# Kernel optimization log

Hardware: AMD Instinct MI355X
Metric: run time of the kernel (lower is better)

The kernel has to match this reference:

```python
import jax, jax.numpy as jnp
import numpy as np

N_NODES = 100000
N_EDGES = 1250000
D_IN = 64
D_H = 64
D_OUT = 32


def setup_inputs() -> dict:
    key = jax.random.key(0)
    ks = jax.random.split(key, 8)
    x = jax.random.normal(ks[0], (N_NODES, D_IN), dtype=jnp.float32)
    edge_index = jax.random.randint(ks[1], (2, N_EDGES), 0, N_NODES, dtype=jnp.int64)
    s = 0.1
    W1_l = jax.random.normal(ks[2], (D_H, D_IN), dtype=jnp.float32) * s
    W1_r = jax.random.normal(ks[3], (D_H, D_IN), dtype=jnp.float32) * s
    b1 = jnp.zeros((D_H,), dtype=jnp.float32)
    W2_l = jax.random.normal(ks[4], (D_OUT, D_H), dtype=jnp.float32) * s
    W2_r = jax.random.normal(ks[5], (D_OUT, D_H), dtype=jnp.float32) * s
    b2 = jnp.zeros((D_OUT,), dtype=jnp.float32)
    return {"x": x, "edge_index": edge_index, "W1_l": W1_l, "W1_r": W1_r,
            "b1": b1, "W2_l": W2_l, "W2_r": W2_r, "b2": b2}


def _sage_conv(x, src, dst, W_l, W_r, b):
    # PyG SAGEConv (aggr='mean', root_weight=True):
    #   out = lin_l(mean_{j in N(i)} x_j) + lin_r(x_i)
    n = x.shape[0]
    msg = x[src]                                            # [E, d] gather
    ssum = jax.ops.segment_sum(msg, dst, num_segments=n)    # [N, d]
    deg = jax.ops.segment_sum(jnp.ones((src.shape[0], 1), x.dtype), dst,
                              num_segments=n)               # [N, 1]
    mean = ssum / jnp.maximum(deg, 1.0)
    return mean @ W_l.T + b + x @ W_r.T


def reference(x, edge_index, W1_l, W1_r, b1, W2_l, W2_r, b2):
    src = edge_index[0]
    dst = edge_index[1]
    h = jax.nn.relu(_sage_conv(x, src, dst, W1_l, W1_r, b1))
    out = _sage_conv(h, src, dst, W2_l, W2_r, b2)
    return out
```

## Files before the change

### kernel.cpp

```cpp
#include <hip/hip_runtime.h>

#define N_NODES 100000
#define N_EDGES 1250000
#define D_IN 64
#define D_H 64
#define D_OUT 32

#define BUCKETS 196
#define GRP 512
#define PREP_NB 512
#define PREP_CH 2442
#define SCAP 48
#define BSTRIDE (PREP_NB*SCAP)
#define CSRCAP 8192

typedef __attribute__((ext_vector_type(8))) short bf16x8;
typedef __attribute__((ext_vector_type(4))) float f32x4;

__device__ __forceinline__ unsigned short f2bf(float f) {
    unsigned u = __float_as_uint(f);
    u = (u + 0x7fffu + ((u >> 16) & 1u)) >> 16;
    return (unsigned short)u;
}
__device__ __forceinline__ float bfhi(unsigned v) { return __uint_as_float(v & 0xffff0000u); }
__device__ __forceinline__ float bflo(unsigned v) { return __uint_as_float(v << 16); }


__global__ __launch_bounds__(256) void k_prep(const float* __restrict__ x,
                                              unsigned short* __restrict__ xh,
                                              const int* __restrict__ src,
                                              const int* __restrict__ dst,
                                              int* __restrict__ ebuf,
                                              int* __restrict__ pcnt) {
    __shared__ int ofs[BUCKETS];
    int t = threadIdx.x, b = blockIdx.x;
    for (int i = t; i < BUCKETS; i += 256) ofs[i] = 0;
    __syncthreads();

    const int TOT = N_NODES * 64 / 4;
    for (int i = b * 256 + t; i < TOT; i += PREP_NB * 256) {
        float4 v = *(const float4*)(x + (size_t)i * 4);
        uint2 u;
        u.x = (unsigned)f2bf(v.x) | ((unsigned)f2bf(v.y) << 16);
        u.y = (unsigned)f2bf(v.z) | ((unsigned)f2bf(v.w) << 16);
        *(uint2*)(xh + (size_t)i * 4) = u;
    }

    int e0 = b * PREP_CH;
    int e1 = e0 + PREP_CH; if (e1 > N_EDGES) e1 = N_EDGES;
    for (int e = e0 + t; e < e1; e += 256) {
        int s = src[e], d = dst[e];
        if ((unsigned)d >= N_NODES) continue;
        int sv = ((unsigned)s < N_NODES) ? s : 0;
        int bk = d >> 9;
        int r = atomicAdd(&ofs[bk], 1);
        if (r < SCAP) ebuf[bk * BSTRIDE + b * SCAP + r] = ((d & 511) << 17) | sv;
    }
    __syncthreads();
    for (int i = t; i < BUCKETS; i += 256) {
        int v = ofs[i]; if (v > SCAP) v = SCAP;
        pcnt[i * PREP_NB + b] = v;
    }
}

__global__ __launch_bounds__(512) void k_phb(const int* __restrict__ ebuf,
                                             const int* __restrict__ pcnt,
                                             int2* __restrict__ rd,
                                             int* __restrict__ csr_src) {
    __shared__ int sedge[CSRCAP];
    __shared__ int cnt[GRP];
    __shared__ int wsum[8];
    int b = blockIdx.x, t = threadIdx.x;
    int lane = t & 63, w = t >> 6;

    cnt[t] = 0;
    int c = pcnt[b * PREP_NB + t];

    int run = c;
    #pragma unroll
    for (int off = 1; off < 64; off <<= 1) {
        int u = __shfl_up(run, off, 64);
        if (lane >= off) run += u;
    }
    if (lane == 63) wsum[w] = run;
    __syncthreads();
    int wbase = 0, tot = 0;
    #pragma unroll
    for (int i = 0; i < 8; ++i) { int v = wsum[i]; tot += v; if (i < w) wbase += v; }
    int base = wbase + run - c;
    int n = tot; if (n > CSRCAP) n = CSRCAP;

    {
        const int4* sp4 = (const int4*)(ebuf + (size_t)b * BSTRIDE + (size_t)t * SCAP);
        for (int j = 0; j < c; j += 4) {
            int4 v = sp4[j >> 2];
            int p = base + j;
            if (p + 0 < CSRCAP)          sedge[p + 0] = v.x;
            if (j + 1 < c && p + 1 < CSRCAP) sedge[p + 1] = v.y;
            if (j + 2 < c && p + 2 < CSRCAP) sedge[p + 2] = v.z;
            if (j + 3 < c && p + 3 < CSRCAP) sedge[p + 3] = v.w;
        }
    }
    __syncthreads();
    for (int i = t; i < n; i += 512) atomicAdd(&cnt[sedge[i] >> 17], 1);
    __syncthreads();

    int d = cnt[t];
    int rund = d;
    #pragma unroll
    for (int off = 1; off < 64; off <<= 1) {
        int u = __shfl_up(rund, off, 64);
        if (lane >= off) rund += u;
    }
    if (lane == 63) wsum[w] = rund;
    __syncthreads();
    int wb2 = 0;
    #pragma unroll
    for (int i = 0; i < 8; ++i) { if (i < w) wb2 += wsum[i]; }
    int gabs = b * CSRCAP + wb2 + rund - d;
    int node = b * GRP + t;
    if (node < N_NODES) rd[node] = make_int2(gabs, d);
    cnt[t] = gabs;
    __syncthreads();
    for (int i = t; i < n; i += 512) {
        int v = sedge[i];
        int pos = atomicAdd(&cnt[v >> 17], 1);
        csr_src[pos] = v & 0x1FFFF;
    }
}

__global__ __launch_bounds__(256) void k_gather1(
    const unsigned short* __restrict__ xh,
    const int2* __restrict__ rd,
    const int* __restrict__ csr_src,
    unsigned int* __restrict__ meanh)
{
    int lane = threadIdx.x & 63;
    int wv = threadIdx.x >> 6;
    int c = lane & 31;
    int hb = lane & 32;
    const unsigned* xp = (const unsigned*)xh;

    int node0 = blockIdx.x * 8 + wv * 2 + (hb >> 5);
    for (int row = node0; row < N_NODES; row += gridDim.x * 8) {
        int2 rdv = rd[row];
        int start = rdv.x, dg = rdv.y;
        int end = start + dg;
        float x0 = 0.f, y0 = 0.f, x1 = 0.f, y1 = 0.f;
        float x2 = 0.f, y2 = 0.f, x3 = 0.f, y3 = 0.f;
        float x4 = 0.f, y4 = 0.f, x5 = 0.f, y5 = 0.f;
        float x6 = 0.f, y6 = 0.f, x7 = 0.f, y7 = 0.f;
        for (int eb = start; eb < end; eb += 32) {
            int nv = end - eb; if (nv > 32) nv = 32;
            int sid = (c < nv) ? csr_src[eb + c] : 0;
            int j = 0;
            for (; j + 8 <= nv; j += 8) {
                int s0 = __shfl(sid, hb + j + 0, 64);
                int s1 = __shfl(sid, hb + j + 1, 64);
                int s2 = __shfl(sid, hb + j + 2, 64);
                int s3 = __shfl(sid, hb + j + 3, 64);
                int s4 = __shfl(sid, hb + j + 4, 64);
                int s5 = __shfl(sid, hb + j + 5, 64);
                int s6 = __shfl(sid, hb + j + 6, 64);
                int s7 = __shfl(sid, hb + j + 7, 64);
                unsigned v0 = xp[s0 * 32 + c];
                unsigned v1 = xp[s1 * 32 + c];
                unsigned v2 = xp[s2 * 32 + c];
                unsigned v3 = xp[s3 * 32 + c];
                unsigned v4 = xp[s4 * 32 + c];
                unsigned v5 = xp[s5 * 32 + c];
                unsigned v6 = xp[s6 * 32 + c];
                unsigned v7 = xp[s7 * 32 + c];
                x0 += bflo(v0); y0 += bfhi(v0);
                x1 += bflo(v1); y1 += bfhi(v1);
                x2 += bflo(v2); y2 += bfhi(v2);
                x3 += bflo(v3); y3 += bfhi(v3);
                x4 += bflo(v4); y4 += bfhi(v4);
                x5 += bflo(v5); y5 += bfhi(v5);
                x6 += bflo(v6); y6 += bfhi(v6);
                x7 += bflo(v7); y7 += bfhi(v7);
            }
            for (; j + 4 <= nv; j += 4) {
                int s0 = __shfl(sid, hb + j + 0, 64);
                int s1 = __shfl(sid, hb + j + 1, 64);
                int s2 = __shfl(sid, hb + j + 2, 64);
                int s3 = __shfl(sid, hb + j + 3, 64);
                unsigned v0 = xp[s0 * 32 + c];
                unsigned v1 = xp[s1 * 32 + c];
                unsigned v2 = xp[s2 * 32 + c];
                unsigned v3 = xp[s3 * 32 + c];
                x0 += bflo(v0); y0 += bfhi(v0);
                x1 += bflo(v1); y1 += bfhi(v1);
                x2 += bflo(v2); y2 += bfhi(v2);
                x3 += bflo(v3); y3 += bfhi(v3);
            }
            for (; j < nv; ++j) {
                int s = __shfl(sid, hb + j, 64);
                unsigned v = xp[s * 32 + c];
                x0 += bflo(v); y0 += bfhi(v);
            }
        }
        float rdeg = 1.0f / fmaxf((float)dg, 1.0f);
        float fx = (((x0 + x1) + (x2 + x3)) + ((x4 + x5) + (x6 + x7))) * rdeg;
        float fy = (((y0 + y1) + (y2 + y3)) + ((y4 + y5) + (y6 + y7))) * rdeg;
        meanh[(size_t)row * 32 + c] = (unsigned)f2bf(fx) | ((unsigned)f2bf(fy) << 16);
    }
}

__global__ __launch_bounds__(256) void k_gemm1(
    const unsigned short* __restrict__ xh, const unsigned short* __restrict__ meanh,
    const float* __restrict__ W1l, const float* __restrict__ W1r,
    const float* __restrict__ b1,
    const float* __restrict__ W2l, const float* __restrict__ W2r,
    unsigned short* __restrict__ hWlh, unsigned short* __restrict__ hrh)
{
    __shared__ short sWB1[4 * 4 * 64 * 8];
    __shared__ short sWB2[2 * 4 * 64 * 8];
    __shared__ short htile[4][16 * 72];

    int tid = threadIdx.x;
    for (int e = tid; e < 1024; e += 256) {
        int kc = e >> 8, nt = (e >> 6) & 3, ln = e & 63;
        int cc = ln & 15, qd = ln >> 4;
        int n = nt * 16 + cc, k0 = kc * 32 + qd * 8;
        const float* sp = (k0 < 64) ? (W1l + n * 64 + k0) : (W1r + n * 64 + (k0 - 64));
        short* dp = sWB1 + e * 8;
        #pragma unroll
        for (int j = 0; j < 8; ++j) dp[j] = (short)f2bf(sp[j]);
    }
    for (int e = tid; e < 512; e += 256) {
        int kc = e >> 8, nt = (e >> 6) & 3, ln = e & 63;
        int cc = ln & 15, qd = ln >> 4;
        int n = nt * 16 + cc, k0 = kc * 32 + qd * 8;
        const float* sp = (n < 32) ? (W2l + n * 64 + k0) : (W2r + (n - 32) * 64 + k0);
        short* dp = sWB2 + e * 8;
        #pragma unroll
        for (int j = 0; j < 8; ++j) dp[j] = (short)f2bf(sp[j]);
    }
    __syncthreads();

    int lane = tid & 63, w = tid >> 6;
    int c = lane & 15, quad = lane >> 4;
    float bias[4];
    #pragma unroll
    for (int nt = 0; nt < 4; ++nt) bias[nt] = b1[nt * 16 + c];

    const bf16x8* B1 = (const bf16x8*)sWB1;
    const bf16x8* B2 = (const bf16x8*)sWB2;
    short* ht = htile[w];

    for (int r0 = blockIdx.x * 64 + w * 16; r0 < N_NODES; r0 += gridDim.x * 64) {
        int ra = r0 + c; if (ra > N_NODES - 1) ra = N_NODES - 1;
        const bf16x8* mrow = (const bf16x8*)(meanh + (size_t)ra * 64);
        const bf16x8* xrow = (const bf16x8*)(xh + (size_t)ra * 64);
        bf16x8 a0 = mrow[quad];
        bf16x8 a1 = mrow[4 + quad];
        bf16x8 a2 = xrow[quad];
        bf16x8 a3 = xrow[4 + quad];

        f32x4 acc[4];
        #pragma unroll
        for (int nt = 0; nt < 4; ++nt) acc[nt] = (f32x4){0.f, 0.f, 0.f, 0.f};
        #pragma unroll
        for (int nt = 0; nt < 4; ++nt)
            acc[nt] = __builtin_amdgcn_mfma_f32_16x16x32_bf16(a0, B1[(0 * 4 + nt) * 64 + lane], acc[nt], 0, 0, 0);
        #pragma unroll
        for (int nt = 0; nt < 4; ++nt)
            acc[nt] = __builtin_amdgcn_mfma_f32_16x16x32_bf16(a1, B1[(1 * 4 + nt) * 64 + lane], acc[nt], 0, 0, 0);
        #pragma unroll
        for (int nt = 0; nt < 4; ++nt)
            acc[nt] = __builtin_amdgcn_mfma_f32_16x16x32_bf16(a2, B1[(2 * 4 + nt) * 64 + lane], acc[nt], 0, 0, 0);
        #pragma unroll
        for (int nt = 0; nt < 4; ++nt)
            acc[nt] = __builtin_amdgcn_mfma_f32_16x16x32_bf16(a3, B1[(3 * 4 + nt) * 64 + lane], acc[nt], 0, 0, 0);

        #pragma unroll
        for (int nt = 0; nt < 4; ++nt) {
            #pragma unroll
            for (int reg = 0; reg < 4; ++reg) {
                float hv = fmaxf(acc[nt][reg] + bias[nt], 0.0f);
                ht[(quad * 4 + reg) * 72 + nt * 16 + c] = (short)f2bf(hv);
            }
        }
        bf16x8 h0 = *(const bf16x8*)(ht + c * 72 + 0  + quad * 8);
        bf16x8 h1 = *(const bf16x8*)(ht + c * 72 + 32 + quad * 8);

        f32x4 acc2[4];
        #pragma unroll
        for (int nt = 0; nt < 4; ++nt) acc2[nt] = (f32x4){0.f, 0.f, 0.f, 0.f};
        #pragma unroll
        for (int nt = 0; nt < 4; ++nt)
            acc2[nt] = __builtin_amdgcn_mfma_f32_16x16x32_bf16(h0, B2[(0 * 4 + nt) * 64 + lane], acc2[nt], 0, 0, 0);
        #pragma unroll
        for (int nt = 0; nt < 4; ++nt)
            acc2[nt] = __builtin_amdgcn_mfma_f32_16x16x32_bf16(h1, B2[(1 * 4 + nt) * 64 + lane], acc2[nt], 0, 0, 0);

        #pragma unroll
        for (int nt = 0; nt < 4; ++nt) {
            #pragma unroll
            for (int reg = 0; reg < 4; ++reg) {
                int row = r0 + quad * 4 + reg;
                if (row < N_NODES) {
                    unsigned short q = f2bf(acc2[nt][reg]);
                    if (nt < 2) hWlh[(size_t)row * 32 + nt * 16 + c] = q;
                    else        hrh [(size_t)row * 32 + (nt - 2) * 16 + c] = q;
                }
            }
        }
    }
}

__global__ __launch_bounds__(256) void k_l2(
    const unsigned short* __restrict__ hWlh, const unsigned short* __restrict__ hrh,
    const int2* __restrict__ rd,
    const int* __restrict__ csr_src,
    const float* __restrict__ b2, float* __restrict__ out)
{
    int lane = threadIdx.x & 63;
    int wv = threadIdx.x >> 6;
    int c = lane & 15;
    int qb = lane & 48;
    const unsigned* hp  = (const unsigned*)hWlh;
    const unsigned* hrp = (const unsigned*)hrh;
    float2 b2v = ((const float2*)b2)[c];

    int node0 = blockIdx.x * 16 + wv * 4 + (qb >> 4);
    for (int row = node0; row < N_NODES; row += gridDim.x * 16) {
        int2 rdv = rd[row];
        int start = rdv.x, dg = rdv.y;
        int end = start + dg;
        float x0 = 0.f, y0 = 0.f, x1 = 0.f, y1 = 0.f;
        float x2 = 0.f, y2 = 0.f, x3 = 0.f, y3 = 0.f;
        float x4 = 0.f, y4 = 0.f, x5 = 0.f, y5 = 0.f;
        float x6 = 0.f, y6 = 0.f, x7 = 0.f, y7 = 0.f;
        for (int eb = start; eb < end; eb += 16) {
            int nv = end - eb; if (nv > 16) nv = 16;
            int sid = (c < nv) ? csr_src[eb + c] : 0;
            int j = 0;
            for (; j + 8 <= nv; j += 8) {
                int s0 = __shfl(sid, qb + j + 0, 64);
                int s1 = __shfl(sid, qb + j + 1, 64);
                int s2 = __shfl(sid, qb + j + 2, 64);
                int s3 = __shfl(sid, qb + j + 3, 64);
                int s4 = __shfl(sid, qb + j + 4, 64);
                int s5 = __shfl(sid, qb + j + 5, 64);
                int s6 = __shfl(sid, qb + j + 6, 64);
                int s7 = __shfl(sid, qb + j + 7, 64);
                unsigned v0 = hp[s0 * 16 + c];
                unsigned v1 = hp[s1 * 16 + c];
                unsigned v2 = hp[s2 * 16 + c];
                unsigned v3 = hp[s3 * 16 + c];
                unsigned v4 = hp[s4 * 16 + c];
                unsigned v5 = hp[s5 * 16 + c];
                unsigned v6 = hp[s6 * 16 + c];
                unsigned v7 = hp[s7 * 16 + c];
                x0 += bflo(v0); y0 += bfhi(v0);
                x1 += bflo(v1); y1 += bfhi(v1);
                x2 += bflo(v2); y2 += bfhi(v2);
                x3 += bflo(v3); y3 += bfhi(v3);
                x4 += bflo(v4); y4 += bfhi(v4);
                x5 += bflo(v5); y5 += bfhi(v5);
                x6 += bflo(v6); y6 += bfhi(v6);
                x7 += bflo(v7); y7 += bfhi(v7);
            }
            for (; j + 4 <= nv; j += 4) {
                int s0 = __shfl(sid, qb + j + 0, 64);
                int s1 = __shfl(sid, qb + j + 1, 64);
                int s2 = __shfl(sid, qb + j + 2, 64);
                int s3 = __shfl(sid, qb + j + 3, 64);
                unsigned v0 = hp[s0 * 16 + c];
                unsigned v1 = hp[s1 * 16 + c];
                unsigned v2 = hp[s2 * 16 + c];
                unsigned v3 = hp[s3 * 16 + c];
                x0 += bflo(v0); y0 += bfhi(v0);
                x1 += bflo(v1); y1 += bfhi(v1);
                x2 += bflo(v2); y2 += bfhi(v2);
                x3 += bflo(v3); y3 += bfhi(v3);
            }
            for (; j < nv; ++j) {
                int s = __shfl(sid, qb + j, 64);
                unsigned v = hp[s * 16 + c];
                x0 += bflo(v); y0 += bfhi(v);
            }
        }
        float fx = ((x0 + x1) + (x2 + x3)) + ((x4 + x5) + (x6 + x7));
        float fy = ((y0 + y1) + (y2 + y3)) + ((y4 + y5) + (y6 + y7));
        float rdeg = 1.0f / fmaxf((float)dg, 1.0f);
        unsigned hru = hrp[(size_t)row * 16 + c];
        float2 o;
        o.x = fmaf(fx, rdeg, bflo(hru) + b2v.x);
        o.y = fmaf(fy, rdeg, bfhi(hru) + b2v.y);
        ((float2*)out)[(size_t)row * 16 + c] = o;
    }
}

extern "C" void kernel_launch(void* const* d_in, const int* in_sizes, int n_in,
                              void* d_out, int out_size, void* d_ws, size_t ws_size,
                              hipStream_t stream) {
    const float* x   = (const float*)d_in[0];
    const int*   ei  = (const int*)d_in[1];
    const float* W1l = (const float*)d_in[2];
    const float* W1r = (const float*)d_in[3];
    const float* b1  = (const float*)d_in[4];
    const float* W2l = (const float*)d_in[5];
    const float* W2r = (const float*)d_in[6];
    const float* b2  = (const float*)d_in[7];
    float* out = (float*)d_out;

    const int* src = ei;
    const int* dst = ei + N_EDGES;

    char* w = (char*)d_ws;
    int2* rd     = (int2*)w;  w += sizeof(int2) * (N_NODES + 4);
    int* pcnt    = (int*)w;   w += sizeof(int) * (PREP_NB * BUCKETS);
    int* csr_src = (int*)w;   w += sizeof(int) * (BUCKETS * CSRCAP);
    int* ebuf    = (int*)w;   w += sizeof(int) * ((size_t)BUCKETS * BSTRIDE);
    unsigned short* xh    = (unsigned short*)w; w += sizeof(short) * (size_t)N_NODES * 64;
    unsigned int*   meanh = (unsigned int*)w;   w += sizeof(int)   * (size_t)N_NODES * 32;
    unsigned short* hWlh  = (unsigned short*)w; w += sizeof(short) * (size_t)N_NODES * 32;
    unsigned short* hrh   = (unsigned short*)w;

    k_prep<<<PREP_NB, 256, 0, stream>>>(x, xh, src, dst, ebuf, pcnt);
    k_phb<<<BUCKETS, 512, 0, stream>>>(ebuf, pcnt, rd, csr_src);
    k_gather1<<<4096, 256, 0, stream>>>(xh, rd, csr_src, meanh);
    k_gemm1<<<(N_NODES + 63) / 64, 256, 0, stream>>>(
        xh, (const unsigned short*)meanh, W1l, W1r, b1, W2l, W2r, hWlh, hrh);
    k_l2<<<4096, 256, 0, stream>>>(hWlh, hrh, rd, csr_src, b2, out);
}
```

Baseline: 195.7 us.

## Quantize gathered node features to int8 with per-row scales for both aggregations

Per-row int8 quantization (offset by 128, with an fp32 scale) replaces the bf16 copies of x and of h·W2_l that the two neighbor-gather kernels read. Each gathered row shrinks from 128 to 64 bytes in layer 1 and from 64 to 32 bytes in layer 2, and the lane mapping is regrouped so each lane dequantizes four values per load. The intent is to cut random-access gather bandwidth, which dominates these kernels. In exchange it adds an extra per-edge scale load and shuffle, extra integer-to-float conversion arithmetic, and coarser 8-bit precision in the aggregated means.

```diff
diff --git a/kernel.cpp b/kernel.cpp
--- a/kernel.cpp
+++ b/kernel.cpp
@@ -28,6 +28,8 @@
 
 __global__ __launch_bounds__(256) void k_prep(const float* __restrict__ x,
                                               unsigned short* __restrict__ xh,
+                                              unsigned* __restrict__ xq,
+                                              float* __restrict__ xscale,
                                               const int* __restrict__ src,
                                               const int* __restrict__ dst,
                                               int* __restrict__ ebuf,
@@ -37,13 +39,25 @@
     for (int i = t; i < BUCKETS; i += 256) ofs[i] = 0;
     __syncthreads();
 
-    const int TOT = N_NODES * 64 / 4;
-    for (int i = b * 256 + t; i < TOT; i += PREP_NB * 256) {
-        float4 v = *(const float4*)(x + (size_t)i * 4);
-        uint2 u;
-        u.x = (unsigned)f2bf(v.x) | ((unsigned)f2bf(v.y) << 16);
-        u.y = (unsigned)f2bf(v.z) | ((unsigned)f2bf(v.w) << 16);
-        *(uint2*)(xh + (size_t)i * 4) = u;
+    int ql = t & 15;
+    for (int row = b * 16 + (t >> 4); row < N_NODES; row += PREP_NB * 16) {
+        float4 v = *(const float4*)(x + (size_t)row * 64 + ql * 4);
+        float amax = fmaxf(fmaxf(fabsf(v.x), fabsf(v.y)), fmaxf(fabsf(v.z), fabsf(v.w)));
+        amax = fmaxf(amax, __shfl_xor(amax, 1, 64));
+        amax = fmaxf(amax, __shfl_xor(amax, 2, 64));
+        amax = fmaxf(amax, __shfl_xor(amax, 4, 64));
+        amax = fmaxf(amax, __shfl_xor(amax, 8, 64));
+        float sinv = (amax > 0.f) ? 127.0f / amax : 0.f;
+        unsigned q0 = (unsigned)((int)rintf(v.x * sinv) + 128);
+        unsigned q1 = (unsigned)((int)rintf(v.y * sinv) + 128);
+        unsigned q2 = (unsigned)((int)rintf(v.z * sinv) + 128);
+        unsigned q3 = (unsigned)((int)rintf(v.w * sinv) + 128);
+        xq[(size_t)row * 16 + ql] = q0 | (q1 << 8) | (q2 << 16) | (q3 << 24);
+        if (ql == 0) xscale[row] = (amax > 0.f) ? amax / 127.0f : 0.f;
+        uint2 hb;
+        hb.x = (unsigned)f2bf(v.x) | ((unsigned)f2bf(v.y) << 16);
+        hb.y = (unsigned)f2bf(v.z) | ((unsigned)f2bf(v.w) << 16);
+        ((uint2*)xh)[(size_t)row * 16 + ql] = hb;
     }
 
     int e0 = b * PREP_CH;
@@ -95,7 +109,7 @@
         for (int j = 0; j < c; j += 4) {
             int4 v = sp4[j >> 2];
             int p = base + j;
-            if (p + 0 < CSRCAP)          sedge[p + 0] = v.x;
+            if (p + 0 < CSRCAP)              sedge[p + 0] = v.x;
             if (j + 1 < c && p + 1 < CSRCAP) sedge[p + 1] = v.y;
             if (j + 2 < c && p + 2 < CSRCAP) sedge[p + 2] = v.z;
             if (j + 3 < c && p + 3 < CSRCAP) sedge[p + 3] = v.w;
@@ -130,80 +144,79 @@
 }
 
 __global__ __launch_bounds__(256) void k_gather1(
-    const unsigned short* __restrict__ xh,
-    const int2* __restrict__ rd,
-    const int* __restrict__ csr_src,
-    unsigned int* __restrict__ meanh)
+    const unsigned* __restrict__ xq, const float* __restrict__ xscale,
+    const int2* __restrict__ rd, const int* __restrict__ csr_src,
+    uint2* __restrict__ meanh)
 {
     int lane = threadIdx.x & 63;
     int wv = threadIdx.x >> 6;
-    int c = lane & 31;
-    int hb = lane & 32;
-    const unsigned* xp = (const unsigned*)xh;
-
-    int node0 = blockIdx.x * 8 + wv * 2 + (hb >> 5);
-    for (int row = node0; row < N_NODES; row += gridDim.x * 8) {
+    int c = lane & 15;
+    int qb = lane & 48;
+
+    int node0 = blockIdx.x * 16 + wv * 4 + (qb >> 4);
+    for (int row = node0; row < N_NODES; row += gridDim.x * 16) {
         int2 rdv = rd[row];
         int start = rdv.x, dg = rdv.y;
         int end = start + dg;
-        float x0 = 0.f, y0 = 0.f, x1 = 0.f, y1 = 0.f;
-        float x2 = 0.f, y2 = 0.f, x3 = 0.f, y3 = 0.f;
-        float x4 = 0.f, y4 = 0.f, x5 = 0.f, y5 = 0.f;
-        float x6 = 0.f, y6 = 0.f, x7 = 0.f, y7 = 0.f;
-        for (int eb = start; eb < end; eb += 32) {
-            int nv = end - eb; if (nv > 32) nv = 32;
-            int sid = (c < nv) ? csr_src[eb + c] : 0;
+        float A0=0,A1=0,A2=0,A3=0, B0=0,B1=0,B2=0,B3=0;
+        float C0=0,C1=0,C2=0,C3=0, D0=0,D1=0,D2=0,D3=0;
+        float ss0=0, ss1=0, ss2=0, ss3=0;
+        for (int eb = start; eb < end; eb += 16) {
+            int nv = end - eb; if (nv > 16) nv = 16;
+            int sid = 0; float sc = 0.f;
+            if (c < nv) { sid = csr_src[eb + c]; sc = xscale[sid]; }
             int j = 0;
-            for (; j + 8 <= nv; j += 8) {
-                int s0 = __shfl(sid, hb + j + 0, 64);
-                int s1 = __shfl(sid, hb + j + 1, 64);
-                int s2 = __shfl(sid, hb + j + 2, 64);
-                int s3 = __shfl(sid, hb + j + 3, 64);
-                int s4 = __shfl(sid, hb + j + 4, 64);
-                int s5 = __shfl(sid, hb + j + 5, 64);
-                int s6 = __shfl(sid, hb + j + 6, 64);
-                int s7 = __shfl(sid, hb + j + 7, 64);
-                unsigned v0 = xp[s0 * 32 + c];
-                unsigned v1 = xp[s1 * 32 + c];
-                unsigned v2 = xp[s2 * 32 + c];
-                unsigned v3 = xp[s3 * 32 + c];
-                unsigned v4 = xp[s4 * 32 + c];
-                unsigned v5 = xp[s5 * 32 + c];
-                unsigned v6 = xp[s6 * 32 + c];
-                unsigned v7 = xp[s7 * 32 + c];
-                x0 += bflo(v0); y0 += bfhi(v0);
-                x1 += bflo(v1); y1 += bfhi(v1);
-                x2 += bflo(v2); y2 += bfhi(v2);
-                x3 += bflo(v3); y3 += bfhi(v3);
-                x4 += bflo(v4); y4 += bfhi(v4);
-                x5 += bflo(v5); y5 += bfhi(v5);
-                x6 += bflo(v6); y6 += bfhi(v6);
-                x7 += bflo(v7); y7 += bfhi(v7);
-            }
             for (; j + 4 <= nv; j += 4) {
-                int s0 = __shfl(sid, hb + j + 0, 64);
-                int s1 = __shfl(sid, hb + j + 1, 64);
-                int s2 = __shfl(sid, hb + j + 2, 64);
-                int s3 = __shfl(sid, hb + j + 3, 64);
-                unsigned v0 = xp[s0 * 32 + c];
-                unsigned v1 = xp[s1 * 32 + c];
-                unsigned v2 = xp[s2 * 32 + c];
-                unsigned v3 = xp[s3 * 32 + c];
-                x0 += bflo(v0); y0 += bfhi(v0);
-                x1 += bflo(v1); y1 += bfhi(v1);
-                x2 += bflo(v2); y2 += bfhi(v2);
-                x3 += bflo(v3); y3 += bfhi(v3);
+                int s0 = __shfl(sid, qb + j + 0, 64); float f0 = __shfl(sc, qb + j + 0, 64);
+                int s1 = __shfl(sid, qb + j + 1, 64); float f1 = __shfl(sc, qb + j + 1, 64);
+                int s2 = __shfl(sid, qb + j + 2, 64); float f2 = __shfl(sc, qb + j + 2, 64);
+                int s3 = __shfl(sid, qb + j + 3, 64); float f3 = __shfl(sc, qb + j + 3, 64);
+                unsigned v0 = xq[(size_t)s0 * 16 + c];
+                unsigned v1 = xq[(size_t)s1 * 16 + c];
+                unsigned v2 = xq[(size_t)s2 * 16 + c];
+                unsigned v3 = xq[(size_t)s3 * 16 + c];
+                A0 = fmaf(f0, (float)(v0 & 255u), A0);
+                A1 = fmaf(f0, (float)((v0 >> 8) & 255u), A1);
+                A2 = fmaf(f0, (float)((v0 >> 16) & 255u), A2);
+                A3 = fmaf(f0, (float)(v0 >> 24), A3);
+                ss0 += f0;
+                B0 = fmaf(f1, (float)(v1 & 255u), B0);
+                B1 = fmaf(f1, (float)((v1 >> 8) & 255u), B1);
+                B2 = fmaf(f1, (float)((v1 >> 16) & 255u), B2);
+                B3 = fmaf(f1, (float)(v1 >> 24), B3);
+                ss1 += f1;
+                C0 = fmaf(f2, (float)(v2 & 255u), C0);
+                C1 = fmaf(f2, (float)((v2 >> 8) & 255u), C1);
+                C2 = fmaf(f2, (float)((v2 >> 16) & 255u), C2);
+                C3 = fmaf(f2, (float)(v2 >> 24), C3);
+                ss2 += f2;
+                D0 = fmaf(f3, (float)(v3 & 255u), D0);
+                D1 = fmaf(f3, (float)((v3 >> 8) & 255u), D1);
+                D2 = fmaf(f3, (float)((v3 >> 16) & 255u), D2);
+                D3 = fmaf(f3, (float)(v3 >> 24), D3);
+                ss3 += f3;
             }
             for (; j < nv; ++j) {
-                int s = __shfl(sid, hb + j, 64);
-                unsigned v = xp[s * 32 + c];
-                x0 += bflo(v); y0 += bfhi(v);
+                int s0 = __shfl(sid, qb + j, 64); float f0 = __shfl(sc, qb + j, 64);
+                unsigned v0 = xq[(size_t)s0 * 16 + c];
+                A0 = fmaf(f0, (float)(v0 & 255u), A0);
+                A1 = fmaf(f0, (float)((v0 >> 8) & 255u), A1);
+                A2 = fmaf(f0, (float)((v0 >> 16) & 255u), A2);
+                A3 = fmaf(f0, (float)(v0 >> 24), A3);
+                ss0 += f0;
             }
         }
+        float ssum = (ss0 + ss1) + (ss2 + ss3);
+        float bias = -128.0f * ssum;
         float rdeg = 1.0f / fmaxf((float)dg, 1.0f);
-        float fx = (((x0 + x1) + (x2 + x3)) + ((x4 + x5) + (x6 + x7))) * rdeg;
-        float fy = (((y0 + y1) + (y2 + y3)) + ((y4 + y5) + (y6 + y7))) * rdeg;
-        meanh[(size_t)row * 32 + c] = (unsigned)f2bf(fx) | ((unsigned)f2bf(fy) << 16);
+        float m0 = ((A0 + B0) + (C0 + D0) + bias) * rdeg;
+        float m1 = ((A1 + B1) + (C1 + D1) + bias) * rdeg;
+        float m2 = ((A2 + B2) + (C2 + D2) + bias) * rdeg;
+        float m3 = ((A3 + B3) + (C3 + D3) + bias) * rdeg;
+        uint2 o;
+        o.x = (unsigned)f2bf(m0) | ((unsigned)f2bf(m1) << 16);
+        o.y = (unsigned)f2bf(m2) | ((unsigned)f2bf(m3) << 16);
+        meanh[(size_t)row * 16 + c] = o;
     }
 }
 
@@ -212,7 +225,8 @@
     const float* __restrict__ W1l, const float* __restrict__ W1r,
     const float* __restrict__ b1,
     const float* __restrict__ W2l, const float* __restrict__ W2r,
-    unsigned short* __restrict__ hWlh, unsigned short* __restrict__ hrh)
+    unsigned char* __restrict__ hq, float* __restrict__ hscale,
+    unsigned short* __restrict__ hrh)
 {
     __shared__ short sWB1[4 * 4 * 64 * 8];
     __shared__ short sWB2[2 * 4 * 64 * 8];
@@ -296,101 +310,104 @@
             acc2[nt] = __builtin_amdgcn_mfma_f32_16x16x32_bf16(h1, B2[(1 * 4 + nt) * 64 + lane], acc2[nt], 0, 0, 0);
 
         #pragma unroll
-        for (int nt = 0; nt < 4; ++nt) {
-            #pragma unroll
-            for (int reg = 0; reg < 4; ++reg) {
-                int row = r0 + quad * 4 + reg;
-                if (row < N_NODES) {
-                    unsigned short q = f2bf(acc2[nt][reg]);
-                    if (nt < 2) hWlh[(size_t)row * 32 + nt * 16 + c] = q;
-                    else        hrh [(size_t)row * 32 + (nt - 2) * 16 + c] = q;
-                }
+        for (int reg = 0; reg < 4; ++reg) {
+            float m = fmaxf(fabsf(acc2[0][reg]), fabsf(acc2[1][reg]));
+            m = fmaxf(m, __shfl_xor(m, 1, 64));
+            m = fmaxf(m, __shfl_xor(m, 2, 64));
+            m = fmaxf(m, __shfl_xor(m, 4, 64));
+            m = fmaxf(m, __shfl_xor(m, 8, 64));
+            int row = r0 + quad * 4 + reg;
+            if (row < N_NODES) {
+                float sinv = (m > 0.f) ? 127.0f / m : 0.f;
+                unsigned q0 = (unsigned)((int)rintf(acc2[0][reg] * sinv) + 128);
+                unsigned q1 = (unsigned)((int)rintf(acc2[1][reg] * sinv) + 128);
+                hq[(size_t)row * 32 + c]      = (unsigned char)q0;
+                hq[(size_t)row * 32 + 16 + c] = (unsigned char)q1;
+                if (c == 0) hscale[row] = (m > 0.f) ? m / 127.0f : 0.f;
+                hrh[(size_t)row * 32 + c]      = f2bf(acc2[2][reg]);
+                hrh[(size_t)row * 32 + 16 + c] = f2bf(acc2[3][reg]);
             }
         }
     }
 }
 
 __global__ __launch_bounds__(256) void k_l2(
-    const unsigned short* __restrict__ hWlh, const unsigned short* __restrict__ hrh,
-    const int2* __restrict__ rd,
-    const int* __restrict__ csr_src,
+    const unsigned char* __restrict__ hq, const float* __restrict__ hscale,
+    const unsigned short* __restrict__ hrh,
+    const int2* __restrict__ rd, const int* __restrict__ csr_src,
     const float* __restrict__ b2, float* __restrict__ out)
 {
     int lane = threadIdx.x & 63;
     int wv = threadIdx.x >> 6;
-    int c = lane & 15;
-    int qb = lane & 48;
-    const unsigned* hp  = (const unsigned*)hWlh;
-    const unsigned* hrp = (const unsigned*)hrh;
-    float2 b2v = ((const float2*)b2)[c];
-
-    int node0 = blockIdx.x * 16 + wv * 4 + (qb >> 4);
-    for (int row = node0; row < N_NODES; row += gridDim.x * 16) {
+    int cc = lane & 7;
+    int gb = lane & 56;
+    const unsigned* hp = (const unsigned*)hq;
+    const uint2* hrp = (const uint2*)hrh;
+    float4 b2v = ((const float4*)b2)[cc];
+
+    int node0 = blockIdx.x * 32 + wv * 8 + (gb >> 3);
+    for (int row = node0; row < N_NODES; row += gridDim.x * 32) {
         int2 rdv = rd[row];
         int start = rdv.x, dg = rdv.y;
         int end = start + dg;
-        float x0 = 0.f, y0 = 0.f, x1 = 0.f, y1 = 0.f;
-        float x2 = 0.f, y2 = 0.f, x3 = 0.f, y3 = 0.f;
-        float x4 = 0.f, y4 = 0.f, x5 = 0.f, y5 = 0.f;
-        float x6 = 0.f, y6 = 0.f, x7 = 0.f, y7 = 0.f;
-        for (int eb = start; eb < end; eb += 16) {
-            int nv = end - eb; if (nv > 16) nv = 16;
-            int sid = (c < nv) ? csr_src[eb + c] : 0;
+        float A0=0,A1=0,A2=0,A3=0, B0=0,B1=0,B2=0,B3=0;
+        float C0=0,C1=0,C2=0,C3=0, D0=0,D1=0,D2=0,D3=0;
+        float ss0=0, ss1=0, ss2=0, ss3=0;
+        for (int eb = start; eb < end; eb += 8) {
+            int nv = end - eb; if (nv > 8) nv = 8;
+            int sid = 0; float sc = 0.f;
+            if (cc < nv) { sid = csr_src[eb + cc]; sc = hscale[sid]; }
             int j = 0;
-            for (; j + 8 <= nv; j += 8) {
-                int s0 = __shfl(sid, qb + j + 0, 64);
-                int s1 = __shfl(sid, qb + j + 1, 64);
-                int s2 = __shfl(sid, qb + j + 2, 64);
-                int s3 = __shfl(sid, qb + j + 3, 64);
-                int s4 = __shfl(sid, qb + j + 4, 64);
-                int s5 = __shfl(sid, qb + j + 5, 64);
-                int s6 = __shfl(sid, qb + j + 6, 64);
-                int s7 = __shfl(sid, qb + j + 7, 64);
-                unsigned v0 = hp[s0 * 16 + c];
-                unsigned v1 = hp[s1 * 16 + c];
-                unsigned v2 = hp[s2 * 16 + c];
-                unsigned v3 = hp[s3 * 16 + c];
-                unsigned v4 = hp[s4 * 16 + c];
-                unsigned v5 = hp[s5 * 16 + c];
-                unsigned v6 = hp[s6 * 16 + c];
-                unsigned v7 = hp[s7 * 16 + c];
-                x0 += bflo(v0); y0 += bfhi(v0);
-                x1 += bflo(v1); y1 += bfhi(v1);
-                x2 += bflo(v2); y2 += bfhi(v2);
-                x3 += bflo(v3); y3 += bfhi(v3);
-                x4 += bflo(v4); y4 += bfhi(v4);
-                x5 += bflo(v5); y5 += bfhi(v5);
-                x6 += bflo(v6); y6 += bfhi(v6);
-                x7 += bflo(v7); y7 += bfhi(v7);
-            }
             for (; j + 4 <= nv; j += 4) {
-                int s0 = __shfl(sid, qb + j + 0, 64);
-                int s1 = __shfl(sid, qb + j + 1, 64);
-                int s2 = __shfl(sid, qb + j + 2, 64);
-                int s3 = __shfl(sid, qb + j + 3, 64);
-                unsigned v0 = hp[s0 * 16 + c];
-                unsigned v1 = hp[s1 * 16 + c];
-                unsigned v2 = hp[s2 * 16 + c];
-                unsigned v3 = hp[s3 * 16 + c];
-                x0 += bflo(v0); y0 += bfhi(v0);
-                x1 += bflo(v1); y1 += bfhi(v1);
-                x2 += bflo(v2); y2 += bfhi(v2);
-                x3 += bflo(v3); y3 += bfhi(v3);
+                int s0 = __shfl(sid, gb + j + 0, 64); float f0 = __shfl(sc, gb + j + 0, 64);
+                int s1 = __shfl(sid, gb + j + 1, 64); float f1 = __shfl(sc, gb + j + 1, 64);
+                int s2 = __shfl(sid, gb + j + 2, 64); float f2 = __shfl(sc, gb + j + 2, 64);
+                int s3 = __shfl(sid, gb + j + 3, 64); float f3 = __shfl(sc, gb + j + 3, 64);
+                unsigned v0 = hp[(size_t)s0 * 8 + cc];
+                unsigned v1 = hp[(size_t)s1 * 8 + cc];
+                unsigned v2 = hp[(size_t)s2 * 8 + cc];
+                unsigned v3 = hp[(size_t)s3 * 8 + cc];
+                A0 = fmaf(f0, (float)(v0 & 255u), A0);
+                A1 = fmaf(f0, (float)((v0 >> 8) & 255u), A1);
+                A2 = fmaf(f0, (float)((v0 >> 16) & 255u), A2);
+                A3 = fmaf(f0, (float)(v0 >> 24), A3);
+                ss0 += f0;
+                B0 = fmaf(f1, (float)(v1 & 255u), B0);
+                B1 = fmaf(f1, (float)((v1 >> 8) & 255u), B1);
+                B2 = fmaf(f1, (float)((v1 >> 16) & 255u), B2);
+                B3 = fmaf(f1, (float)(v1 >> 24), B3);
+                ss1 += f1;
+                C0 = fmaf(f2, (float)(v2 & 255u), C0);
+                C1 = fmaf(f2, (float)((v2 >> 8) & 255u), C1);
+                C2 = fmaf(f2, (float)((v2 >> 16) & 255u), C2);
+                C3 = fmaf(f2, (float)(v2 >> 24), C3);
+                ss2 += f2;
+                D0 = fmaf(f3, (float)(v3 & 255u), D0);
+                D1 = fmaf(f3, (float)((v3 >> 8) & 255u), D1);
+                D2 = fmaf(f3, (float)((v3 >> 16) & 255u), D2);
+                D3 = fmaf(f3, (float)(v3 >> 24), D3);
+                ss3 += f3;
             }
             for (; j < nv; ++j) {
-                int s = __shfl(sid, qb + j, 64);
-                unsigned v = hp[s * 16 + c];
-                x0 += bflo(v); y0 += bfhi(v);
+                int s0 = __shfl(sid, gb + j, 64); float f0 = __shfl(sc, gb + j, 64);
+                unsigned v0 = hp[(size_t)s0 * 8 + cc];
+                A0 = fmaf(f0, (float)(v0 & 255u), A0);
+                A1 = fmaf(f0, (float)((v0 >> 8) & 255u), A1);
+                A2 = fmaf(f0, (float)((v0 >> 16) & 255u), A2);
+                A3 = fmaf(f0, (float)(v0 >> 24), A3);
+                ss0 += f0;
             }
         }
-        float fx = ((x0 + x1) + (x2 + x3)) + ((x4 + x5) + (x6 + x7));
-        float fy = ((y0 + y1) + (y2 + y3)) + ((y4 + y5) + (y6 + y7));
+        float ssum = (ss0 + ss1) + (ss2 + ss3);
+        float bias = -128.0f * ssum;
         float rdeg = 1.0f / fmaxf((float)dg, 1.0f);
-        unsigned hru = hrp[(size_t)row * 16 + c];
-        float2 o;
-        o.x = fmaf(fx, rdeg, bflo(hru) + b2v.x);
-        o.y = fmaf(fy, rdeg, bfhi(hru) + b2v.y);
-        ((float2*)out)[(size_t)row * 16 + c] = o;
+        uint2 hru = hrp[(size_t)row * 8 + cc];
+        float4 o;
+        o.x = fmaf((A0 + B0) + (C0 + D0) + bias, rdeg, bflo(hru.x) + b2v.x);
+        o.y = fmaf((A1 + B1) + (C1 + D1) + bias, rdeg, bfhi(hru.x) + b2v.y);
+        o.z = fmaf((A2 + B2) + (C2 + D2) + bias, rdeg, bflo(hru.y) + b2v.z);
+        o.w = fmaf((A3 + B3) + (C3 + D3) + bias, rdeg, bfhi(hru.y) + b2v.w);
+        ((float4*)out)[(size_t)row * 8 + cc] = o;
     }
 }
 
@@ -415,15 +432,18 @@
     int* pcnt    = (int*)w;   w += sizeof(int) * (PREP_NB * BUCKETS);
     int* csr_src = (int*)w;   w += sizeof(int) * (BUCKETS * CSRCAP);
     int* ebuf    = (int*)w;   w += sizeof(int) * ((size_t)BUCKETS * BSTRIDE);
-    unsigned short* xh    = (unsigned short*)w; w += sizeof(short) * (size_t)N_NODES * 64;
-    unsigned int*   meanh = (unsigned int*)w;   w += sizeof(int)   * (size_t)N_NODES * 32;
-    unsigned short* hWlh  = (unsigned short*)w; w += sizeof(short) * (size_t)N_NODES * 32;
-    unsigned short* hrh   = (unsigned short*)w;
-
-    k_prep<<<PREP_NB, 256, 0, stream>>>(x, xh, src, dst, ebuf, pcnt);
+    unsigned short* xh   = (unsigned short*)w; w += sizeof(short) * (size_t)N_NODES * 64;
+    unsigned*       xq   = (unsigned*)w;       w += sizeof(int)   * (size_t)N_NODES * 16;
+    float*          xscale = (float*)w;        w += sizeof(float) * (N_NODES + 8);
+    unsigned*       meanh  = (unsigned*)w;     w += sizeof(int)   * (size_t)N_NODES * 32;
+    unsigned char*  hq   = (unsigned char*)w;  w += (size_t)N_NODES * 32;
+    float*          hscale = (float*)w;        w += sizeof(float) * (N_NODES + 8);
+    unsigned short* hrh  = (unsigned short*)w;
+
+    k_prep<<<PREP_NB, 256, 0, stream>>>(x, xh, xq, xscale, src, dst, ebuf, pcnt);
     k_phb<<<BUCKETS, 512, 0, stream>>>(ebuf, pcnt, rd, csr_src);
-    k_gather1<<<4096, 256, 0, stream>>>(xh, rd, csr_src, meanh);
-    k_gemm1<<<(N_NODES + 63) / 64, 256, 0, stream>>>(
-        xh, (const unsigned short*)meanh, W1l, W1r, b1, W2l, W2r, hWlh, hrh);
-    k_l2<<<4096, 256, 0, stream>>>(hWlh, hrh, rd, csr_src, b2, out);
-}
+    k_gather1<<<2048, 256, 0, stream>>>(xq, xscale, rd, csr_src, (uint2*)meanh);
+    k_gemm1<<<1024, 256, 0, stream>>>(
+        xh, (const unsigned short*)meanh, W1l, W1r, b1, W2l, W2r, hq, hscale, hrh);
+    k_l2<<<2048, 256, 0, stream>>>(hq, hscale, hrh, rd, csr_src, b2, out);
+}
```

Result: faster. 190.7 us (-2.5%).
